# Optimization experiments

Hardware: AMD Instinct MI355X
Metric: run time of the kernel (lower is better)

## Reference

```python
import jax, jax.numpy as jnp
import numpy as np

N_OBJ, N_SR, N_V, N_F = 8192, 4096, 4100, 4096
EPS = 1e-8


def setup_inputs() -> dict:
    key = jax.random.key(0)
    k1, k2, k3, k4, k5 = jax.random.split(key, 5)
    obj_points = jax.random.normal(k1, (N_OBJ, 3), jnp.float32)
    sr_points = 0.5 * jax.random.normal(k2, (N_SR, 3), jnp.float32)
    hand_verts = 0.5 * jax.random.normal(k3, (N_V, 3), jnp.float32)
    face_normals = jax.random.normal(k4, (N_F, 3), jnp.float32)
    hand_faces = jax.random.randint(k5, (N_F, 3), 0, N_V)
    return dict(obj_points=obj_points, sr_points=sr_points,
                hand_verts=hand_verts, face_normals=face_normals,
                hand_faces=hand_faces)


def reference(obj_points, sr_points, hand_verts, face_normals, hand_faces):
    # --- get_NN: brute-force nearest hand point for every object point ---
    d2 = (jnp.sum(obj_points**2, -1)[:, None]
          + jnp.sum(sr_points**2, -1)[None, :]
          - 2.0 * obj_points @ sr_points.T)          # [N, M] squared dists
    nn_idx = jnp.argmin(d2, axis=1)                   # [N]
    trg_pts = sr_points[nn_idx]                       # batched_index_select -> [N,3]
    D = trg_pts - obj_points                          # ray directions [N,3]

    # --- ray-triangle intersection (plane test + 3 edge half-plane tests) ---
    # All [F,N,3] intermediates are avoided via triple-product expansion:
    # every quantity reduces to einsums of per-face [F,3] with per-ray [N,3].
    tri = hand_verts[hand_faces]                      # [F,3,3]
    v0, v1, v2 = tri[:, 0], tri[:, 1], tri[:, 2]
    n = face_normals                                  # [F,3]

    denom = jnp.einsum('fk,nk->fn', n, D)             # D . n   [F,N]
    num = jnp.sum(v0 * n, -1)[:, None] - jnp.einsum('fk,nk->fn', n, obj_points)
    dmask = jnp.abs(denom) > EPS
    t = num / jnp.where(dmask, denom, 1.0)            # plane hit parameter [F,N]

    def edge_sign(va, vb):
        # ((vb-va) x (P-va)) . n  with  P = O + t*D, expanded bilinearly
        c = jnp.cross(n, vb - va)                     # [F,3]
        base = (jnp.einsum('fk,nk->fn', c, obj_points)
                - jnp.sum(va * c, -1)[:, None])
        return base + t * jnp.einsum('fk,nk->fn', c, D)

    inside = ((edge_sign(v0, v1) >= 0)
              & (edge_sign(v1, v2) >= 0)
              & (edge_sign(v2, v0) >= 0))
    hit = inside & dmask & (t > EPS)                  # [F,N]

    hit_number = jnp.sum(hit.astype(jnp.int32), axis=0)   # per ray [N]
    interior = (hit_number % 2) != 0                        # odd parity -> inside

    diff = trg_pts - obj_points
    pen_dist = jnp.sqrt(jnp.sum(diff**2 * interior[:, None].astype(diff.dtype)) + 1e-12)

    # --- contact_map_of_m_to_n(obj_points, sr_points) ---
    nn_dist = jnp.sqrt(jnp.maximum(jnp.min(d2, axis=1), 0.0))
    cmap = 1.0 - 2.0 * (jax.nn.sigmoid(100.0 * nn_dist) - 0.5)

    return pen_dist, cmap
```

## Files before the change

### kernel.cpp

```cpp
#include <hip/hip_runtime.h>
#include <math.h>

#define N_OBJ 8192
#define N_SR  4096
#define N_F   4096
#define EPSF  1e-8f
#define EPS2F 1e-16f

typedef float v2f __attribute__((ext_vector_type(2)));
static __device__ __forceinline__ v2f sp(float x) { v2f r; r.x = x; r.y = x; return r; }
static __device__ __forceinline__ v2f vfma(v2f a, v2f b, v2f c) { return __builtin_elementwise_fma(a, b, c); }

__global__ void __launch_bounds__(256) nn_all(const float* __restrict__ obj,
                                              const float* __restrict__ sr,
                                              const float* __restrict__ hv,
                                              const float* __restrict__ fn,
                                              const int* __restrict__ hf,
                                              float* __restrict__ out,
                                              float4* __restrict__ Dws,
                                              float4* __restrict__ F,
                                              int* __restrict__ done) {
    __shared__ float4 cXY[512];
    __shared__ float4 cZS[512];
    const int tid = threadIdx.x, b = blockIdx.x;
    const float2* sr2 = (const float2*)sr;

    if (b == 0 && tid == 0) done[0] = 0;
    if (tid < 4) {
        const int f = b * 4 + tid;
        const int i0 = hf[3*f], i1 = hf[3*f+1], i2 = hf[3*f+2];
        const float v0x = hv[3*i0], v0y = hv[3*i0+1], v0z = hv[3*i0+2];
        const float v1x = hv[3*i1], v1y = hv[3*i1+1], v1z = hv[3*i1+2];
        const float v2x = hv[3*i2], v2y = hv[3*i2+1], v2z = hv[3*i2+2];
        const float nx = fn[3*f], ny = fn[3*f+1], nz = fn[3*f+2];
        F[4*f+0] = make_float4(nx, ny, nz, v0x*nx + v0y*ny + v0z*nz);
        {
            float ex = v1x-v0x, ey = v1y-v0y, ez = v1z-v0z;
            float cx = ny*ez-nz*ey, cy = nz*ex-nx*ez, cz = nx*ey-ny*ex;
            F[4*f+1] = make_float4(cx, cy, cz, v0x*cx + v0y*cy + v0z*cz);
        }
        {
            float ex = v2x-v1x, ey = v2y-v1y, ez = v2z-v1z;
            float cx = ny*ez-nz*ey, cy = nz*ex-nx*ez, cz = nx*ey-ny*ex;
            F[4*f+2] = make_float4(cx, cy, cz, v1x*cx + v1y*cy + v1z*cz);
        }
        {
            float ex = v0x-v2x, ey = v0y-v2y, ez = v0z-v2z;
            float cx = ny*ez-nz*ey, cy = nz*ex-nx*ez, cz = nx*ey-ny*ex;
            F[4*f+3] = make_float4(cx, cy, cz, v2x*cx + v2y*cy + v2z*cz);
        }
    }

    const int w = tid >> 6, lane = tid & 63;
    const int p0 = b * 8 + w * 2, p1 = p0 + 1;

    const float ax = obj[3*p0], ay = obj[3*p0+1], az = obj[3*p0+2];
    const float bx = obj[3*p1], by = obj[3*p1+1], bz = obj[3*p1+2];
    const float aaa = fmaf(ax, ax, fmaf(ay, ay, az * az));
    const float aab = fmaf(bx, bx, fmaf(by, by, bz * bz));

    float a0 = INFINITY, a1 = INFINITY, c0v = INFINITY, c1v = INFINITY;
    int ai0 = 0, ai1 = 1, ci0 = 0, ci1 = 1;

    for (int c = 0; c < 4; ++c) {
        __syncthreads();
        {
            int e0 = tid, e1 = tid + 256;
#pragma unroll
            for (int t = 0; t < 2; ++t) {
                int e = t ? e1 : e0;
                int gp = c * 512 + e;
                float2 A = sr2[3 * gp], B = sr2[3 * gp + 1], C = sr2[3 * gp + 2];
                float x0 = A.x, y0 = A.y, z0 = B.x, x1 = B.y, y1 = C.x, z1 = C.y;
                cXY[e] = make_float4(x0, x1, y0, y1);
                cZS[e] = make_float4(z0, z1,
                                     fmaf(x0, x0, fmaf(y0, y0, z0 * z0)),
                                     fmaf(x1, x1, fmaf(y1, y1, z1 * z1)));
            }
        }
        __syncthreads();

        int e2 = c * 1024 + lane * 2;
#pragma unroll
        for (int step = 0; step < 8; ++step) {
            int e = step * 64 + lane;
            float4 A = cXY[e];
            float4 B = cZS[e];
            v2f X; X.x = A.x; X.y = A.y;
            v2f Y; Y.x = A.z; Y.y = A.w;
            v2f Z; Z.x = B.x; Z.y = B.y;
            v2f SS; SS.x = B.z; SS.y = B.w;
            {
                v2f d  = vfma(Z, sp(az), vfma(Y, sp(ay), X * sp(ax)));
                v2f d2 = vfma(d, sp(-2.f), SS);
                bool q0 = d2.x < a0, q1 = d2.y < a1;
                a0 = q0 ? d2.x : a0;  ai0 = q0 ? e2     : ai0;
                a1 = q1 ? d2.y : a1;  ai1 = q1 ? e2 + 1 : ai1;
            }
            {
                v2f d  = vfma(Z, sp(bz), vfma(Y, sp(by), X * sp(bx)));
                v2f d2 = vfma(d, sp(-2.f), SS);
                bool q0 = d2.x < c0v, q1 = d2.y < c1v;
                c0v = q0 ? d2.x : c0v;  ci0 = q0 ? e2     : ci0;
                c1v = q1 ? d2.y : c1v;  ci1 = q1 ? e2 + 1 : ci1;
            }
            e2 += 128;
        }
    }

    float bdA = a0; int biA = ai0;
    if (a1 < bdA || (a1 == bdA && ai1 < biA)) { bdA = a1; biA = ai1; }
    float bdB = c0v; int biB = ci0;
    if (c1v < bdB || (c1v == bdB && ci1 < biB)) { bdB = c1v; biB = ci1; }
#pragma unroll
    for (int off = 32; off > 0; off >>= 1) {
        float d = __shfl_down(bdA, off);
        int   i = __shfl_down(biA, off);
        if (d < bdA || (d == bdA && i < biA)) { bdA = d; biA = i; }
        float e = __shfl_down(bdB, off);
        int   j = __shfl_down(biB, off);
        if (e < bdB || (e == bdB && j < biB)) { bdB = e; biB = j; }
    }
    if (lane == 0) {
        {
            float dx = sr[3*biA] - ax, dy = sr[3*biA+1] - ay, dz = sr[3*biA+2] - az;
            Dws[p0] = make_float4(dx, dy, dz, fmaf(dx, dx, fmaf(dy, dy, dz * dz)));
            float nn  = sqrtf(fmaxf(bdA + aaa, 0.f));
            float sig = 1.f / (1.f + expf(-100.f * nn));
            out[1 + p0] = 1.f - 2.f * (sig - 0.5f);
        }
        {
            float dx = sr[3*biB] - bx, dy = sr[3*biB+1] - by, dz = sr[3*biB+2] - bz;
            Dws[p1] = make_float4(dx, dy, dz, fmaf(dx, dx, fmaf(dy, dy, dz * dz)));
            float nn  = sqrtf(fmaxf(bdB + aab, 0.f));
            float sig = 1.f / (1.f + expf(-100.f * nn));
            out[1 + p1] = 1.f - 2.f * (sig - 0.5f);
        }
    }
}

#define RFC 64
__global__ void __launch_bounds__(256) ray_count(const float* __restrict__ obj,
                                                 const float4* __restrict__ Dws,
                                                 const float4* __restrict__ F,
                                                 unsigned char* __restrict__ pcount) {
    __shared__ float4 sF[RFC * 4];
    const int tid = threadIdx.x;
    const int pg = blockIdx.x & 15, fc = blockIdx.x >> 4;

    sF[tid] = (F + (size_t)fc * RFC * 4)[tid];

    float px[2], py[2], pz[2], qx[2], qy[2], qz[2];
    int cnt[2];
#pragma unroll
    for (int h = 0; h < 2; ++h) {
        int p = pg * 512 + h * 256 + tid;
        px[h] = obj[3*p]; py[h] = obj[3*p+1]; pz[h] = obj[3*p+2];
        float4 D = Dws[p];
        qx[h] = D.x; qy[h] = D.y; qz[h] = D.z;
        cnt[h] = 0;
    }
    __syncthreads();

    float4 nF0 = sF[0], nF1 = sF[1], nF2 = sF[2], nF3 = sF[3];
#pragma unroll 4
    for (int f = 0; f < RFC; ++f) {
        const float4 Fn = nF0, C1 = nF1, C2 = nF2, C3 = nF3;
        if (f + 1 < RFC) {
            nF0 = sF[4*f+4]; nF1 = sF[4*f+5]; nF2 = sF[4*f+6]; nF3 = sF[4*f+7];
        }
#pragma unroll
        for (int h = 0; h < 2; ++h) {
            float denom = fmaf(Fn.z, qz[h], fmaf(Fn.y, qy[h], Fn.x * qx[h]));
            float num   = Fn.w - fmaf(Fn.z, pz[h], fmaf(Fn.y, py[h], Fn.x * px[h]));
            float d2 = denom * denom;
            float nd = num * denom;
            float wx = fmaf(px[h], d2, nd * qx[h]);
            float wy = fmaf(py[h], d2, nd * qy[h]);
            float wz = fmaf(pz[h], d2, nd * qz[h]);
            float q1 = fmaf(-C1.w, d2, fmaf(C1.z, wz, fmaf(C1.y, wy, C1.x * wx)));
            float q2 = fmaf(-C2.w, d2, fmaf(C2.z, wz, fmaf(C2.y, wy, C2.x * wx)));
            float q3 = fmaf(-C3.w, d2, fmaf(C3.z, wz, fmaf(C3.y, wy, C3.x * wx)));
            float tc = fmaf(-EPSF, d2, nd);
            float dc = d2 - EPS2F;
            float m  = fminf(fminf(q1, q2), fminf(q3, fminf(tc, dc)));
            cnt[h] += (m >= 0.f) ? 1 : 0;
        }
    }
#pragma unroll
    for (int h = 0; h < 2; ++h)
        pcount[(size_t)fc * N_OBJ + pg * 512 + h * 256 + tid] = (unsigned char)cnt[h];
}

#define NCH (N_F / RFC)
__global__ void __launch_bounds__(256) finalize(const float4* __restrict__ Dws,
                                                const unsigned char* __restrict__ pcount,
                                                float* __restrict__ fpart,
                                                int* __restrict__ done,
                                                float* __restrict__ out) {
    __shared__ float wsum[4];
    const int tid = threadIdx.x;
    const int pt = blockIdx.x * 256 + tid;

    int c = 0;
#pragma unroll 8
    for (int fc = 0; fc < NCH; ++fc)
        c += pcount[(size_t)fc * N_OBJ + pt];
    float s = (c & 1) ? Dws[pt].w : 0.f;
#pragma unroll
    for (int off = 32; off > 0; off >>= 1) s += __shfl_down(s, off);
    if ((tid & 63) == 0) wsum[tid >> 6] = s;
    __syncthreads();
    if (tid == 0) {
        fpart[blockIdx.x] = wsum[0] + wsum[1] + wsum[2] + wsum[3];
        __threadfence();
        if (atomicAdd(done, 1) == 31) {
            float tot = 0.f;
            for (int i = 0; i < 32; ++i)
                tot += atomicAdd(&fpart[i], 0.f);
            out[0] = sqrtf(tot + 1e-12f);
        }
    }
}

extern "C" void kernel_launch(void* const* d_in, const int* in_sizes, int n_in,
                              void* d_out, int out_size, void* d_ws, size_t ws_size,
                              hipStream_t stream) {
    const float* obj = (const float*)d_in[0];
    const float* sr  = (const float*)d_in[1];
    const float* hv  = (const float*)d_in[2];
    const float* fn  = (const float*)d_in[3];
    const int*   hf  = (const int*)d_in[4];
    float* out = (float*)d_out;

    char* ws = (char*)d_ws;
    float4*        Dws    = (float4*)(ws + 0);
    float4*        F      = (float4*)(ws + 131072);
    unsigned char* pcount = (unsigned char*)(ws + 393216);
    float*         fpart  = (float*)(ws + 917504);
    int*           done   = (int*)  (ws + 917632);

    nn_all<<<1024, 256, 0, stream>>>(obj, sr, hv, fn, hf, out, Dws, F, done);
    ray_count<<<1024, 256, 0, stream>>>(obj, Dws, F, pcount);
    finalize<<<32, 256, 0, stream>>>(Dws, pcount, fpart, done, out);
}
```

Measured before the change: 113.5 us.

## Fuse parity finalize into ray_count, process four rays per thread

Each ray_count thread now handles four rays instead of two, so blocks are halved to 512. Per-chunk hit counts are packed as bytes into one 32-bit word, and the separate finalize kernel is replaced by a last-block-done reduction inside ray_count. That last block XORs the packed counts to get parity and sums the squared penetration distances. This removes one kernel launch and reuses each face load across more rays. The cost is higher register pressure, fewer blocks for occupancy, and a serial tail where a single block reduces all 8192 rays.

```diff
diff --git a/kernel.cpp b/kernel.cpp
--- a/kernel.cpp
+++ b/kernel.cpp
@@ -65,10 +65,9 @@
     for (int c = 0; c < 4; ++c) {
         __syncthreads();
         {
-            int e0 = tid, e1 = tid + 256;
 #pragma unroll
             for (int t = 0; t < 2; ++t) {
-                int e = t ? e1 : e0;
+                int e = t * 256 + tid;
                 int gp = c * 512 + e;
                 float2 A = sr2[3 * gp], B = sr2[3 * gp + 1], C = sr2[3 * gp + 2];
                 float x0 = A.x, y0 = A.y, z0 = B.x, x1 = B.y, y1 = C.x, z1 = C.y;
@@ -140,25 +139,38 @@
 }
 
 #define RFC 64
+#define RAY_NB 512
 __global__ void __launch_bounds__(256) ray_count(const float* __restrict__ obj,
                                                  const float4* __restrict__ Dws,
                                                  const float4* __restrict__ F,
-                                                 unsigned char* __restrict__ pcount) {
+                                                 unsigned* __restrict__ pcount32,
+                                                 int* __restrict__ done,
+                                                 float* __restrict__ out) {
     __shared__ float4 sF[RFC * 4];
+    __shared__ float wsum[4];
+    __shared__ int lastf;
     const int tid = threadIdx.x;
-    const int pg = blockIdx.x & 15, fc = blockIdx.x >> 4;
+    const int pg = blockIdx.x & 7, fc = blockIdx.x >> 3;
 
     sF[tid] = (F + (size_t)fc * RFC * 4)[tid];
 
-    float px[2], py[2], pz[2], qx[2], qy[2], qz[2];
-    int cnt[2];
-#pragma unroll
-    for (int h = 0; h < 2; ++h) {
-        int p = pg * 512 + h * 256 + tid;
-        px[h] = obj[3*p]; py[h] = obj[3*p+1]; pz[h] = obj[3*p+2];
-        float4 D = Dws[p];
-        qx[h] = D.x; qy[h] = D.y; qz[h] = D.z;
-        cnt[h] = 0;
+    float px[4], py[4], pz[4], qx[4], qy[4], qz[4];
+    int cnt[4];
+    {
+        const float4* obj4 = (const float4*)obj;
+        int base = pg * 768 + tid * 3;
+        float4 A = obj4[base], B = obj4[base + 1], C = obj4[base + 2];
+        px[0] = A.x; py[0] = A.y; pz[0] = A.z;
+        px[1] = A.w; py[1] = B.x; pz[1] = B.y;
+        px[2] = B.z; py[2] = B.w; pz[2] = C.x;
+        px[3] = C.y; py[3] = C.z; pz[3] = C.w;
+        int p4 = pg * 1024 + tid * 4;
+#pragma unroll
+        for (int h = 0; h < 4; ++h) {
+            float4 D = Dws[p4 + h];
+            qx[h] = D.x; qy[h] = D.y; qz[h] = D.z;
+            cnt[h] = 0;
+        }
     }
     __syncthreads();
 
@@ -170,7 +182,7 @@
             nF0 = sF[4*f+4]; nF1 = sF[4*f+5]; nF2 = sF[4*f+6]; nF3 = sF[4*f+7];
         }
 #pragma unroll
-        for (int h = 0; h < 2; ++h) {
+        for (int h = 0; h < 4; ++h) {
             float denom = fmaf(Fn.z, qz[h], fmaf(Fn.y, qy[h], Fn.x * qx[h]));
             float num   = Fn.w - fmaf(Fn.z, pz[h], fmaf(Fn.y, py[h], Fn.x * px[h]));
             float d2 = denom * denom;
@@ -187,40 +199,40 @@
             cnt[h] += (m >= 0.f) ? 1 : 0;
         }
     }
-#pragma unroll
-    for (int h = 0; h < 2; ++h)
-        pcount[(size_t)fc * N_OBJ + pg * 512 + h * 256 + tid] = (unsigned char)cnt[h];
-}
-
-#define NCH (N_F / RFC)
-__global__ void __launch_bounds__(256) finalize(const float4* __restrict__ Dws,
-                                                const unsigned char* __restrict__ pcount,
-                                                float* __restrict__ fpart,
-                                                int* __restrict__ done,
-                                                float* __restrict__ out) {
-    __shared__ float wsum[4];
-    const int tid = threadIdx.x;
-    const int pt = blockIdx.x * 256 + tid;
-
-    int c = 0;
+    pcount32[(size_t)fc * 2048 + pg * 256 + tid] =
+        (unsigned)cnt[0] | ((unsigned)cnt[1] << 8) |
+        ((unsigned)cnt[2] << 16) | ((unsigned)cnt[3] << 24);
+
+    __syncthreads();
+    if (tid == 0) {
+        __threadfence();
+        lastf = (atomicAdd(done, 1) == RAY_NB - 1) ? 1 : 0;
+    }
+    __syncthreads();
+    if (!lastf) return;
+    __threadfence();
+
+    float s = 0.f;
+#pragma unroll
+    for (int it = 0; it < 8; ++it) {
+        int wi = it * 256 + tid;
+        unsigned x = 0;
 #pragma unroll 8
-    for (int fc = 0; fc < NCH; ++fc)
-        c += pcount[(size_t)fc * N_OBJ + pt];
-    float s = (c & 1) ? Dws[pt].w : 0.f;
+        for (int fcc = 0; fcc < 64; ++fcc)
+            x ^= __hip_atomic_load(&pcount32[fcc * 2048 + wi],
+                                   __ATOMIC_RELAXED, __HIP_MEMORY_SCOPE_AGENT);
+        int p4 = wi * 4;
+        if (x & 0x01u)        s += Dws[p4 + 0].w;
+        if (x & 0x0100u)      s += Dws[p4 + 1].w;
+        if (x & 0x010000u)    s += Dws[p4 + 2].w;
+        if (x & 0x01000000u)  s += Dws[p4 + 3].w;
+    }
 #pragma unroll
     for (int off = 32; off > 0; off >>= 1) s += __shfl_down(s, off);
     if ((tid & 63) == 0) wsum[tid >> 6] = s;
     __syncthreads();
-    if (tid == 0) {
-        fpart[blockIdx.x] = wsum[0] + wsum[1] + wsum[2] + wsum[3];
-        __threadfence();
-        if (atomicAdd(done, 1) == 31) {
-            float tot = 0.f;
-            for (int i = 0; i < 32; ++i)
-                tot += atomicAdd(&fpart[i], 0.f);
-            out[0] = sqrtf(tot + 1e-12f);
-        }
-    }
+    if (tid == 0)
+        out[0] = sqrtf(wsum[0] + wsum[1] + wsum[2] + wsum[3] + 1e-12f);
 }
 
 extern "C" void kernel_launch(void* const* d_in, const int* in_sizes, int n_in,
@@ -234,13 +246,11 @@
     float* out = (float*)d_out;
 
     char* ws = (char*)d_ws;
-    float4*        Dws    = (float4*)(ws + 0);
-    float4*        F      = (float4*)(ws + 131072);
-    unsigned char* pcount = (unsigned char*)(ws + 393216);
-    float*         fpart  = (float*)(ws + 917504);
-    int*           done   = (int*)  (ws + 917632);
+    float4*   Dws      = (float4*)(ws + 0);
+    float4*   F        = (float4*)(ws + 131072);
+    unsigned* pcount32 = (unsigned*)(ws + 393216);
+    int*      done     = (int*)(ws + 917504);
 
     nn_all<<<1024, 256, 0, stream>>>(obj, sr, hv, fn, hf, out, Dws, F, done);
-    ray_count<<<1024, 256, 0, stream>>>(obj, Dws, F, pcount);
-    finalize<<<32, 256, 0, stream>>>(Dws, pcount, fpart, done, out);
+    ray_count<<<RAY_NB, 256, 0, stream>>>(obj, Dws, F, pcount32, done, out);
 }
```

After: 136.3 us. 20.1% more time.
